# Performance work log

Hardware: AMD Instinct MI355X
Metric: run time of the kernel (lower is better)

Reference implementation:

```python
import jax, jax.numpy as jnp
import numpy as np

N = 4096
IN_F = 512
OUT_F = 256
HEADS = 4
HEAD_DIM = OUT_F // HEADS


def setup_inputs() -> dict:
    key = jax.random.key(0)
    k_feat, k_adj, k_w, k_a = jax.random.split(key, 4)
    features = jax.random.normal(k_feat, (N, IN_F), dtype=jnp.float32)
    adj_matrix = jax.random.uniform(k_adj, (N, N), dtype=jnp.float32)
    # xavier-uniform-ish init scaled small
    W = jax.random.normal(k_w, (OUT_F, IN_F), dtype=jnp.float32) * (1.0 / np.sqrt(IN_F))
    a = jax.random.normal(k_a, (HEADS, 2 * HEAD_DIM), dtype=jnp.float32) * 0.1
    bias = jnp.zeros((OUT_F,), dtype=jnp.float32)
    return {"features": features, "adj_matrix": adj_matrix, "W": W, "a": a, "bias": bias}


def reference(features, adj_matrix, W, a, bias):
    n = features.shape[0]
    h = features @ W.T                      # [N, OUT_F]
    hh = h.reshape(n, HEADS, HEAD_DIM)      # [N, H, D]
    # e[i,j,h] = leaky_relu(<h_i, a[:, :D]> + <h_j, a[:, D:]>) -- additive decomposition
    e_src = jnp.einsum('nhd,hd->nh', hh, a[:, :HEAD_DIM])   # [N, H]
    e_dst = jnp.einsum('nhd,hd->nh', hh, a[:, HEAD_DIM:])   # [N, H]
    e = e_src[:, None, :] + e_dst[None, :, :]               # [N, N, H]
    e = jnp.where(e >= 0, e, 0.2 * e)                       # leaky_relu(0.2)
    mask = adj_matrix[:, :, None] > 0.1                     # [N, N, 1]
    e = jnp.where(mask, e, -jnp.inf)
    attention = jax.nn.softmax(e, axis=1)                   # softmax over j
    attention = jnp.nan_to_num(attention, nan=0.0)          # fully-masked rows -> 0
    attention_mean = attention.mean(axis=2)                 # [N, N]
    h_out = attention_mean @ h + bias                       # [N, OUT_F]
    return h_out
```

## Files before the change

### kernel.cpp

```cpp
#include <hip/hip_runtime.h>
#include <math.h>

#define NN      4096
#define INF_    512
#define OUTF    256
#define NHEAD   4
#define HDIM    64

typedef __attribute__((ext_vector_type(8))) short  short8x;
typedef __attribute__((ext_vector_type(4))) float  float4x;

__device__ __forceinline__ unsigned short f2bf(float x) {
    union { float f; unsigned int u; } c; c.f = x;
    unsigned int r = (c.u + 0x7FFFu + ((c.u >> 16) & 1u)) >> 16;
    return (unsigned short)r;
}
__device__ __forceinline__ float bflo(unsigned int u) {
    union { unsigned int x; float f; } c; c.x = u << 16; return c.f;
}
__device__ __forceinline__ float bfhi(unsigned int u) {
    union { unsigned int x; float f; } c; c.x = u & 0xFFFF0000u; return c.f;
}

__global__ __launch_bounds__(256) void k_cast(const float* __restrict__ feat,
                                              const float* __restrict__ W,
                                              unsigned short* __restrict__ featb,
                                              unsigned short* __restrict__ Wb) {
    const int b = blockIdx.x;
    const float* src;
    unsigned short* dst;
    int idx;
    if (b < 2048) { src = feat; dst = featb; idx = b * 1024 + threadIdx.x * 4; }
    else          { src = W;    dst = Wb;    idx = (b - 2048) * 1024 + threadIdx.x * 4; }
    float4x v = *(const float4x*)(src + idx);
    ushort4 u;
    u.x = f2bf(v[0]); u.y = f2bf(v[1]); u.z = f2bf(v[2]); u.w = f2bf(v[3]);
    *(ushort4*)(dst + idx) = u;
}

__global__ __launch_bounds__(256) void k_h_gemm(const unsigned short* __restrict__ featb,
                                                const unsigned short* __restrict__ Wb,
                                                float* __restrict__ h32,
                                                unsigned short* __restrict__ hT) {
    __shared__ __align__(16) unsigned short lds_f[64 * 40];
    __shared__ __align__(16) unsigned short lds_w[64 * 40];
    const int tid  = threadIdx.x;
    const int w    = tid >> 6;
    const int lane = tid & 63;
    const int lidx = lane & 15;
    const int quad = lane >> 4;
    const int o0 = blockIdx.x * 64;
    const int i0 = blockIdx.y * 64;
    const int sr = tid >> 2;
    const int skq = (tid & 3) * 8;

    float4x acc[4];
    #pragma unroll
    for (int nt = 0; nt < 4; ++nt) acc[nt] = (float4x){0.f, 0.f, 0.f, 0.f};

    ushort4 pf0, pf1, pw0, pw1;
    {
        pf0 = *(const ushort4*)&featb[(size_t)(i0 + sr) * INF_ + skq];
        pf1 = *(const ushort4*)&featb[(size_t)(i0 + sr) * INF_ + skq + 4];
        pw0 = *(const ushort4*)&Wb[(size_t)(o0 + sr) * INF_ + skq];
        pw1 = *(const ushort4*)&Wb[(size_t)(o0 + sr) * INF_ + skq + 4];
    }
    for (int kt = 0; kt < INF_; kt += 32) {
        __syncthreads();
        *(ushort4*)&lds_f[sr * 40 + skq]     = pf0;
        *(ushort4*)&lds_f[sr * 40 + skq + 4] = pf1;
        *(ushort4*)&lds_w[sr * 40 + skq]     = pw0;
        *(ushort4*)&lds_w[sr * 40 + skq + 4] = pw1;
        __syncthreads();
        if (kt + 32 < INF_) {
            int kn = kt + 32;
            pf0 = *(const ushort4*)&featb[(size_t)(i0 + sr) * INF_ + kn + skq];
            pf1 = *(const ushort4*)&featb[(size_t)(i0 + sr) * INF_ + kn + skq + 4];
            pw0 = *(const ushort4*)&Wb[(size_t)(o0 + sr) * INF_ + kn + skq];
            pw1 = *(const ushort4*)&Wb[(size_t)(o0 + sr) * INF_ + kn + skq + 4];
        }
        short8x af = *(const short8x*)&lds_f[(w * 16 + lidx) * 40 + quad * 8];
        short8x bw[4];
        #pragma unroll
        for (int t = 0; t < 4; ++t)
            bw[t] = *(const short8x*)&lds_w[(t * 16 + lidx) * 40 + quad * 8];
        #pragma unroll
        for (int nt = 0; nt < 4; ++nt)
            acc[nt] = __builtin_amdgcn_mfma_f32_16x16x32_bf16(af, bw[nt], acc[nt], 0, 0, 0);
    }
    #pragma unroll
    for (int nt = 0; nt < 4; ++nt) {
        int col = o0 + nt * 16 + lidx;
        int m0r = i0 + w * 16 + quad * 4;
        #pragma unroll
        for (int rr = 0; rr < 4; ++rr)
            h32[(size_t)(m0r + rr) * OUTF + col] = acc[nt][rr];
        ushort4 u;
        u.x = f2bf(acc[nt][0]); u.y = f2bf(acc[nt][1]);
        u.z = f2bf(acc[nt][2]); u.w = f2bf(acc[nt][3]);
        *(ushort4*)&hT[(size_t)col * NN + m0r] = u;
    }
}

__global__ __launch_bounds__(256) void k_edge_proj(const float* __restrict__ h32,
                                                   const float* __restrict__ a,
                                                   float* __restrict__ es,
                                                   unsigned short* __restrict__ Bt,
                                                   unsigned short* __restrict__ Dt) {
    const int n = blockIdx.x;
    const int w = threadIdx.x >> 6;
    const int lane = threadIdx.x & 63;
    float v  = h32[(size_t)n * OUTF + w * HDIM + lane];
    float s1 = v * a[w * 2 * HDIM + lane];
    float s2 = v * a[w * 2 * HDIM + HDIM + lane];
    #pragma unroll
    for (int off = 32; off; off >>= 1) {
        s1 += __shfl_down(s1, off);
        s2 += __shfl_down(s2, off);
    }
    if (lane == 0) {
        es[n * NHEAD + w] = s1;
        Bt[n * NHEAD + w] = f2bf(__expf(s2));
        Dt[n * NHEAD + w] = f2bf(__expf(0.2f * s2));
    }
}

__global__ __launch_bounds__(256) void k_den(const float* __restrict__ adj,
                                             const float* __restrict__ es,
                                             const unsigned short* __restrict__ Bt,
                                             const unsigned short* __restrict__ Dt,
                                             float* __restrict__ coefA,
                                             float* __restrict__ coefC) {
    __shared__ float red[2][2][8];
    const int tid = threadIdx.x;
    const int r  = tid >> 7;
    const int l  = tid & 127;
    const int wv = (tid >> 6) & 1;
    const int i  = blockIdx.x * 2 + r;

    const float4x esv = ((const float4x*)es)[i];
    float TB[4];
    #pragma unroll
    for (int h = 0; h < 4; ++h) TB[h] = __expf(-esv[h]);
    const float4x* arow4 = (const float4x*)(adj + (size_t)i * NN);
    const uint4* B4 = (const uint4*)Bt;
    const uint4* D4 = (const uint4*)Dt;

    float S1[4] = {0.f, 0.f, 0.f, 0.f};
    float S2[4] = {0.f, 0.f, 0.f, 0.f};
    #pragma unroll
    for (int it = 0; it < 8; ++it) {
        int jv = it * 128 + l;
        float4x av = arow4[jv];
        uint4 bu0 = B4[jv * 2], bu1 = B4[jv * 2 + 1];
        uint4 du0 = D4[jv * 2], du1 = D4[jv * 2 + 1];
        const unsigned int* bw = (const unsigned int*)&bu0;
        const unsigned int* dw = (const unsigned int*)&du0;
        (void)bu1; (void)du1;
        unsigned int bwv[8] = {bu0.x, bu0.y, bu0.z, bu0.w, bu1.x, bu1.y, bu1.z, bu1.w};
        unsigned int dwv[8] = {du0.x, du0.y, du0.z, du0.w, du1.x, du1.y, du1.z, du1.w};
        (void)bw; (void)dw;
        #pragma unroll
        for (int u = 0; u < 4; ++u) {
            bool m = av[u] > 0.1f;
            float b0 = bflo(bwv[u * 2]), b1 = bfhi(bwv[u * 2]);
            float b2 = bflo(bwv[u * 2 + 1]), b3 = bfhi(bwv[u * 2 + 1]);
            float d0 = bflo(dwv[u * 2]), d1 = bfhi(dwv[u * 2]);
            float d2 = bflo(dwv[u * 2 + 1]), d3 = bfhi(dwv[u * 2 + 1]);
            bool p0 = b0 >= TB[0], p1 = b1 >= TB[1], p2 = b2 >= TB[2], p3 = b3 >= TB[3];
            S1[0] += (m && p0) ? b0 : 0.f;   S2[0] += (m && !p0) ? d0 : 0.f;
            S1[1] += (m && p1) ? b1 : 0.f;   S2[1] += (m && !p1) ? d1 : 0.f;
            S1[2] += (m && p2) ? b2 : 0.f;   S2[2] += (m && !p2) ? d2 : 0.f;
            S1[3] += (m && p3) ? b3 : 0.f;   S2[3] += (m && !p3) ? d3 : 0.f;
        }
    }
    #pragma unroll
    for (int off = 1; off < 64; off <<= 1) {
        #pragma unroll
        for (int h = 0; h < 4; ++h) {
            S1[h] += __shfl_xor(S1[h], off);
            S2[h] += __shfl_xor(S2[h], off);
        }
    }
    if ((tid & 63) == 0) {
        #pragma unroll
        for (int h = 0; h < 4; ++h) { red[r][wv][h] = S1[h]; red[r][wv][4 + h] = S2[h]; }
    }
    __syncthreads();
    if (tid < 8) {
        int rr = tid >> 2, h = tid & 3;
        int ii = blockIdx.x * 2 + rr;
        float s1 = red[rr][0][h] + red[rr][1][h];
        float s2 = red[rr][0][4 + h] + red[rr][1][4 + h];
        float e = es[ii * NHEAD + h];
        float A = __expf(e), C = __expf(0.2f * e);
        float den = A * s1 + C * s2;
        float sc = den > 0.f ? 0.25f / den : 0.f;
        coefA[ii * NHEAD + h] = A * sc;
        coefC[ii * NHEAD + h] = C * sc;
    }
}

__global__ __launch_bounds__(256) void k_write(const float* __restrict__ adj,
                                               const float* __restrict__ es,
                                               const unsigned short* __restrict__ Bt,
                                               const unsigned short* __restrict__ Dt,
                                               const float* __restrict__ coefA,
                                               const float* __restrict__ coefC,
                                               unsigned short* __restrict__ attn) {
    const int tid = threadIdx.x;
    const int r = tid >> 7;
    const int l = tid & 127;
    const int i = blockIdx.x * 2 + r;

    const float4x esv = ((const float4x*)es)[i];
    const float4x cA = ((const float4x*)coefA)[i];
    const float4x cC = ((const float4x*)coefC)[i];
    float TB[4];
    #pragma unroll
    for (int h = 0; h < 4; ++h) TB[h] = __expf(-esv[h]);
    const float4x* arow4 = (const float4x*)(adj + (size_t)i * NN);
    const uint4* B4 = (const uint4*)Bt;
    const uint4* D4 = (const uint4*)Dt;
    unsigned short* orow = attn + (size_t)i * NN;

    #pragma unroll
    for (int it = 0; it < 8; ++it) {
        int jv = it * 128 + l;
        float4x av = arow4[jv];
        uint4 bu0 = B4[jv * 2], bu1 = B4[jv * 2 + 1];
        uint4 du0 = D4[jv * 2], du1 = D4[jv * 2 + 1];
        unsigned int bwv[8] = {bu0.x, bu0.y, bu0.z, bu0.w, bu1.x, bu1.y, bu1.z, bu1.w};
        unsigned int dwv[8] = {du0.x, du0.y, du0.z, du0.w, du1.x, du1.y, du1.z, du1.w};
        ushort4 o;
        unsigned short* op = (unsigned short*)&o;
        #pragma unroll
        for (int u = 0; u < 4; ++u) {
            float b0 = bflo(bwv[u * 2]), b1 = bfhi(bwv[u * 2]);
            float b2 = bflo(bwv[u * 2 + 1]), b3 = bfhi(bwv[u * 2 + 1]);
            float d0 = bflo(dwv[u * 2]), d1 = bfhi(dwv[u * 2]);
            float d2 = bflo(dwv[u * 2 + 1]), d3 = bfhi(dwv[u * 2 + 1]);
            float p;
            p  = (b0 >= TB[0]) ? cA[0] * b0 : cC[0] * d0;
            p += (b1 >= TB[1]) ? cA[1] * b1 : cC[1] * d1;
            p += (b2 >= TB[2]) ? cA[2] * b2 : cC[2] * d2;
            p += (b3 >= TB[3]) ? cA[3] * b3 : cC[3] * d3;
            op[u] = f2bf((av[u] > 0.1f) ? p : 0.f);
        }
        *(ushort4*)&orow[jv * 4] = o;
    }
}

__global__ __launch_bounds__(256) void k_out_gemm(const unsigned short* __restrict__ attn,
                                                  const unsigned short* __restrict__ hT,
                                                  float* __restrict__ partials) {
    __shared__ __align__(16) unsigned short lds_a[64 * 40];
    __shared__ __align__(16) unsigned short lds_h[256 * 40];
    const int tid  = threadIdx.x;
    const int w    = tid >> 6;
    const int lane = tid & 63;
    const int lidx = lane & 15;
    const int quad = lane >> 4;
    const int i0    = blockIdx.x * 64;
    const int kbase = blockIdx.y * (NN / 4);
    const int srow = tid >> 3;
    const int skq  = tid & 7;

    float4x acc[4][4];
    #pragma unroll
    for (int a = 0; a < 4; ++a)
        #pragma unroll
        for (int b = 0; b < 4; ++b)
            acc[a][b] = (float4x){0.f, 0.f, 0.f, 0.f};

    ushort4 pa[2], ph[8];
    #pragma unroll
    for (int it = 0; it < 2; ++it)
        pa[it] = *(const ushort4*)&attn[(size_t)(i0 + it * 32 + srow) * NN + kbase + skq * 4];
    #pragma unroll
    for (int it = 0; it < 8; ++it)
        ph[it] = *(const ushort4*)&hT[(size_t)(it * 32 + srow) * NN + kbase + skq * 4];

    for (int ks = 0; ks < 32; ++ks) {
        __syncthreads();
        #pragma unroll
        for (int it = 0; it < 2; ++it)
            *(ushort4*)&lds_a[(it * 32 + srow) * 40 + skq * 4] = pa[it];
        #pragma unroll
        for (int it = 0; it < 8; ++it)
            *(ushort4*)&lds_h[(it * 32 + srow) * 40 + skq * 4] = ph[it];
        __syncthreads();
        if (ks < 31) {
            const int ktn = kbase + (ks + 1) * 32;
            #pragma unroll
            for (int it = 0; it < 2; ++it)
                pa[it] = *(const ushort4*)&attn[(size_t)(i0 + it * 32 + srow) * NN + ktn + skq * 4];
            #pragma unroll
            for (int it = 0; it < 8; ++it)
                ph[it] = *(const ushort4*)&hT[(size_t)(it * 32 + srow) * NN + ktn + skq * 4];
        }
        short8x af[4], bfr[4];
        #pragma unroll
        for (int t = 0; t < 4; ++t) {
            af[t]  = *(const short8x*)&lds_a[(t * 16 + lidx) * 40 + quad * 8];
            bfr[t] = *(const short8x*)&lds_h[(w * 64 + t * 16 + lidx) * 40 + quad * 8];
        }
        #pragma unroll
        for (int it = 0; it < 4; ++it)
            #pragma unroll
            for (int nt = 0; nt < 4; ++nt)
                acc[it][nt] = __builtin_amdgcn_mfma_f32_16x16x32_bf16(
                    af[it], bfr[nt], acc[it][nt], 0, 0, 0);
    }
    float* pbase = partials + (size_t)blockIdx.y * NN * OUTF;
    #pragma unroll
    for (int it = 0; it < 4; ++it)
        #pragma unroll
        for (int nt = 0; nt < 4; ++nt)
            #pragma unroll
            for (int rr = 0; rr < 4; ++rr) {
                int row = i0 + it * 16 + quad * 4 + rr;
                int col = w * 64 + nt * 16 + lidx;
                pbase[(size_t)row * OUTF + col] = acc[it][nt][rr];
            }
}

__global__ __launch_bounds__(256) void k_reduce_out(const float* __restrict__ partials,
                                                    const float* __restrict__ bias,
                                                    float* __restrict__ out) {
    const int i = blockIdx.x;
    const int n = threadIdx.x;
    float acc = bias[n];
    #pragma unroll
    for (int s = 0; s < 4; ++s)
        acc += partials[((size_t)s * NN + i) * OUTF + n];
    out[(size_t)i * OUTF + n] = acc;
}

extern "C" void kernel_launch(void* const* d_in, const int* in_sizes, int n_in,
                              void* d_out, int out_size, void* d_ws, size_t ws_size,
                              hipStream_t stream) {
    const float* feat = (const float*)d_in[0];
    const float* adj  = (const float*)d_in[1];
    const float* W    = (const float*)d_in[2];
    const float* a    = (const float*)d_in[3];
    const float* bias = (const float*)d_in[4];
    float* out = (float*)d_out;

    char* ws = (char*)d_ws;
    float*          es    = (float*)(ws + 0);
    unsigned short* Btb   = (unsigned short*)(ws + (64u << 10));
    unsigned short* Dtb   = (unsigned short*)(ws + (96u << 10));
    float*          coefA = (float*)(ws + (128u << 10));
    float*          coefC = (float*)(ws + (192u << 10));
    unsigned short* hT    = (unsigned short*)(ws + (256u << 10));
    unsigned short* attn  = (unsigned short*)(ws + (2560u << 10));
    unsigned short* featb = (unsigned short*)(ws + (2560u << 10));
    unsigned short* Wb    = (unsigned short*)(ws + (6656u << 10));
    float*          h32   = (float*)(ws + (7168u << 10));
    float*          partials = (float*)(ws + (35328u << 10));

    k_cast      <<<2176,        256, 0, stream>>>(feat, W, featb, Wb);
    k_h_gemm    <<<dim3(4, 64), 256, 0, stream>>>(featb, Wb, h32, hT);
    k_edge_proj <<<NN,          256, 0, stream>>>(h32, a, es, Btb, Dtb);
    k_den       <<<2048,        256, 0, stream>>>(adj, es, Btb, Dtb, coefA, coefC);
    k_write     <<<2048,        256, 0, stream>>>(adj, es, Btb, Dtb, coefA, coefC, attn);
    k_out_gemm  <<<dim3(64, 4), 256, 0, stream>>>(attn, hT, partials);
    k_reduce_out<<<NN,          256, 0, stream>>>(partials, bias, out);
}
```

Measured before the change: 190.0 us.

## Fold attention vector into W, fuse denominator and write passes, deepen split-K

Precomputes W^T·a per head so the edge scores come straight from the features, dropping the fp32 h buffer and the separate edge-projection kernel. Merges the softmax-denominator and attention-write kernels into one, keeping the coefficients in shared memory, so the coefA/coefC global round trip and one launch go away. Doubles the split-K factor of the output GEMM to 8 for more parallelism, at the cost of a larger partials reduction. The edge scores now use fp32 features rather than h, which slightly changes the rounding of the scores.

Measured after the change: 184.0 us. 3.2% less time.

```diff
diff --git a/kernel.cpp b/kernel.cpp
--- a/kernel.cpp
+++ b/kernel.cpp
@@ -6,6 +6,7 @@
 #define OUTF    256
 #define NHEAD   4
 #define HDIM    64
+#define KSPLIT  8
 
 typedef __attribute__((ext_vector_type(8))) short  short8x;
 typedef __attribute__((ext_vector_type(4))) float  float4x;
@@ -22,25 +23,78 @@
     union { unsigned int x; float f; } c; c.x = u & 0xFFFF0000u; return c.f;
 }
 
-__global__ __launch_bounds__(256) void k_cast(const float* __restrict__ feat,
+__global__ __launch_bounds__(256) void k_prep(const float* __restrict__ feat,
                                               const float* __restrict__ W,
+                                              const float* __restrict__ a,
                                               unsigned short* __restrict__ featb,
-                                              unsigned short* __restrict__ Wb) {
+                                              unsigned short* __restrict__ Wb,
+                                              float* __restrict__ wsrc,
+                                              float* __restrict__ wdst) {
     const int b = blockIdx.x;
+    if (b < 8) {
+        const int kk = threadIdx.x & 63, h = threadIdx.x >> 6;
+        const int k = b * 64 + kk;
+        float s = 0.f, d2 = 0.f;
+        #pragma unroll 8
+        for (int d = 0; d < 64; ++d) {
+            float wv = W[(size_t)(h * HDIM + d) * INF_ + k];
+            s  += wv * a[h * 2 * HDIM + d];
+            d2 += wv * a[h * 2 * HDIM + HDIM + d];
+        }
+        wsrc[k * NHEAD + h] = s;
+        wdst[k * NHEAD + h] = d2;
+        return;
+    }
+    const int bb = b - 8;
     const float* src;
     unsigned short* dst;
     int idx;
-    if (b < 2048) { src = feat; dst = featb; idx = b * 1024 + threadIdx.x * 4; }
-    else          { src = W;    dst = Wb;    idx = (b - 2048) * 1024 + threadIdx.x * 4; }
+    if (bb < 2048) { src = feat; dst = featb; idx = bb * 1024 + threadIdx.x * 4; }
+    else           { src = W;    dst = Wb;    idx = (bb - 2048) * 1024 + threadIdx.x * 4; }
     float4x v = *(const float4x*)(src + idx);
     ushort4 u;
     u.x = f2bf(v[0]); u.y = f2bf(v[1]); u.z = f2bf(v[2]); u.w = f2bf(v[3]);
     *(ushort4*)(dst + idx) = u;
 }
 
+__global__ __launch_bounds__(256) void k_edge(const float* __restrict__ feat,
+                                              const float* __restrict__ wsrc,
+                                              const float* __restrict__ wdst,
+                                              float* __restrict__ es,
+                                              unsigned short* __restrict__ Bt,
+                                              unsigned short* __restrict__ Dt) {
+    const int r = blockIdx.x * 16 + (threadIdx.x >> 4);
+    const int lane = threadIdx.x & 15;
+    float s[4] = {0.f, 0.f, 0.f, 0.f};
+    float d[4] = {0.f, 0.f, 0.f, 0.f};
+    for (int kk = 0; kk < 32; ++kk) {
+        int k = kk * 16 + lane;
+        float f = feat[(size_t)r * INF_ + k];
+        float4x ws = ((const float4x*)wsrc)[k];
+        float4x wd = ((const float4x*)wdst)[k];
+        #pragma unroll
+        for (int h = 0; h < 4; ++h) { s[h] += f * ws[h]; d[h] += f * wd[h]; }
+    }
+    #pragma unroll
+    for (int off = 1; off < 16; off <<= 1) {
+        #pragma unroll
+        for (int h = 0; h < 4; ++h) {
+            s[h] += __shfl_xor(s[h], off);
+            d[h] += __shfl_xor(d[h], off);
+        }
+    }
+    if (lane == 0) {
+        #pragma unroll
+        for (int h = 0; h < 4; ++h) {
+            es[r * NHEAD + h] = s[h];
+            Bt[r * NHEAD + h] = f2bf(__expf(d[h]));
+            Dt[r * NHEAD + h] = f2bf(__expf(0.2f * d[h]));
+        }
+    }
+}
+
 __global__ __launch_bounds__(256) void k_h_gemm(const unsigned short* __restrict__ featb,
                                                 const unsigned short* __restrict__ Wb,
-                                                float* __restrict__ h32,
                                                 unsigned short* __restrict__ hT) {
     __shared__ __align__(16) unsigned short lds_f[64 * 40];
     __shared__ __align__(16) unsigned short lds_w[64 * 40];
@@ -58,13 +112,11 @@
     #pragma unroll
     for (int nt = 0; nt < 4; ++nt) acc[nt] = (float4x){0.f, 0.f, 0.f, 0.f};
 
-    ushort4 pf0, pf1, pw0, pw1;
-    {
-        pf0 = *(const ushort4*)&featb[(size_t)(i0 + sr) * INF_ + skq];
-        pf1 = *(const ushort4*)&featb[(size_t)(i0 + sr) * INF_ + skq + 4];
-        pw0 = *(const ushort4*)&Wb[(size_t)(o0 + sr) * INF_ + skq];
-        pw1 = *(const ushort4*)&Wb[(size_t)(o0 + sr) * INF_ + skq + 4];
-    }
+    ushort4 pf0 = *(const ushort4*)&featb[(size_t)(i0 + sr) * INF_ + skq];
+    ushort4 pf1 = *(const ushort4*)&featb[(size_t)(i0 + sr) * INF_ + skq + 4];
+    ushort4 pw0 = *(const ushort4*)&Wb[(size_t)(o0 + sr) * INF_ + skq];
+    ushort4 pw1 = *(const ushort4*)&Wb[(size_t)(o0 + sr) * INF_ + skq + 4];
+
     for (int kt = 0; kt < INF_; kt += 32) {
         __syncthreads();
         *(ushort4*)&lds_f[sr * 40 + skq]     = pf0;
@@ -92,9 +144,6 @@
     for (int nt = 0; nt < 4; ++nt) {
         int col = o0 + nt * 16 + lidx;
         int m0r = i0 + w * 16 + quad * 4;
-        #pragma unroll
-        for (int rr = 0; rr < 4; ++rr)
-            h32[(size_t)(m0r + rr) * OUTF + col] = acc[nt][rr];
         ushort4 u;
         u.x = f2bf(acc[nt][0]); u.y = f2bf(acc[nt][1]);
         u.z = f2bf(acc[nt][2]); u.w = f2bf(acc[nt][3]);
@@ -102,36 +151,13 @@
     }
 }
 
-__global__ __launch_bounds__(256) void k_edge_proj(const float* __restrict__ h32,
-                                                   const float* __restrict__ a,
-                                                   float* __restrict__ es,
-                                                   unsigned short* __restrict__ Bt,
-                                                   unsigned short* __restrict__ Dt) {
-    const int n = blockIdx.x;
-    const int w = threadIdx.x >> 6;
-    const int lane = threadIdx.x & 63;
-    float v  = h32[(size_t)n * OUTF + w * HDIM + lane];
-    float s1 = v * a[w * 2 * HDIM + lane];
-    float s2 = v * a[w * 2 * HDIM + HDIM + lane];
-    #pragma unroll
-    for (int off = 32; off; off >>= 1) {
-        s1 += __shfl_down(s1, off);
-        s2 += __shfl_down(s2, off);
-    }
-    if (lane == 0) {
-        es[n * NHEAD + w] = s1;
-        Bt[n * NHEAD + w] = f2bf(__expf(s2));
-        Dt[n * NHEAD + w] = f2bf(__expf(0.2f * s2));
-    }
-}
-
-__global__ __launch_bounds__(256) void k_den(const float* __restrict__ adj,
-                                             const float* __restrict__ es,
-                                             const unsigned short* __restrict__ Bt,
-                                             const unsigned short* __restrict__ Dt,
-                                             float* __restrict__ coefA,
-                                             float* __restrict__ coefC) {
+__global__ __launch_bounds__(256) void k_attn(const float* __restrict__ adj,
+                                              const float* __restrict__ es,
+                                              const unsigned short* __restrict__ Bt,
+                                              const unsigned short* __restrict__ Dt,
+                                              unsigned short* __restrict__ attn) {
     __shared__ float red[2][2][8];
+    __shared__ float cfs[2][8];
     const int tid = threadIdx.x;
     const int r  = tid >> 7;
     const int l  = tid & 127;
@@ -154,12 +180,8 @@
         float4x av = arow4[jv];
         uint4 bu0 = B4[jv * 2], bu1 = B4[jv * 2 + 1];
         uint4 du0 = D4[jv * 2], du1 = D4[jv * 2 + 1];
-        const unsigned int* bw = (const unsigned int*)&bu0;
-        const unsigned int* dw = (const unsigned int*)&du0;
-        (void)bu1; (void)du1;
         unsigned int bwv[8] = {bu0.x, bu0.y, bu0.z, bu0.w, bu1.x, bu1.y, bu1.z, bu1.w};
         unsigned int dwv[8] = {du0.x, du0.y, du0.z, du0.w, du1.x, du1.y, du1.z, du1.w};
-        (void)bw; (void)dw;
         #pragma unroll
         for (int u = 0; u < 4; ++u) {
             bool m = av[u] > 0.1f;
@@ -196,34 +218,15 @@
         float A = __expf(e), C = __expf(0.2f * e);
         float den = A * s1 + C * s2;
         float sc = den > 0.f ? 0.25f / den : 0.f;
-        coefA[ii * NHEAD + h] = A * sc;
-        coefC[ii * NHEAD + h] = C * sc;
-    }
-}
-
-__global__ __launch_bounds__(256) void k_write(const float* __restrict__ adj,
-                                               const float* __restrict__ es,
-                                               const unsigned short* __restrict__ Bt,
-                                               const unsigned short* __restrict__ Dt,
-                                               const float* __restrict__ coefA,
-                                               const float* __restrict__ coefC,
-                                               unsigned short* __restrict__ attn) {
-    const int tid = threadIdx.x;
-    const int r = tid >> 7;
-    const int l = tid & 127;
-    const int i = blockIdx.x * 2 + r;
-
-    const float4x esv = ((const float4x*)es)[i];
-    const float4x cA = ((const float4x*)coefA)[i];
-    const float4x cC = ((const float4x*)coefC)[i];
-    float TB[4];
-    #pragma unroll
-    for (int h = 0; h < 4; ++h) TB[h] = __expf(-esv[h]);
-    const float4x* arow4 = (const float4x*)(adj + (size_t)i * NN);
-    const uint4* B4 = (const uint4*)Bt;
-    const uint4* D4 = (const uint4*)Dt;
+        cfs[rr][h]     = A * sc;
+        cfs[rr][4 + h] = C * sc;
+    }
+    __syncthreads();
+    float cA[4], cC[4];
+    #pragma unroll
+    for (int h = 0; h < 4; ++h) { cA[h] = cfs[r][h]; cC[h] = cfs[r][4 + h]; }
+
     unsigned short* orow = attn + (size_t)i * NN;
-
     #pragma unroll
     for (int it = 0; it < 8; ++it) {
         int jv = it * 128 + l;
@@ -262,7 +265,7 @@
     const int lidx = lane & 15;
     const int quad = lane >> 4;
     const int i0    = blockIdx.x * 64;
-    const int kbase = blockIdx.y * (NN / 4);
+    const int kbase = blockIdx.y * (NN / KSPLIT);
     const int srow = tid >> 3;
     const int skq  = tid & 7;
 
@@ -281,7 +284,8 @@
     for (int it = 0; it < 8; ++it)
         ph[it] = *(const ushort4*)&hT[(size_t)(it * 32 + srow) * NN + kbase + skq * 4];
 
-    for (int ks = 0; ks < 32; ++ks) {
+    const int KSTEPS = (NN / KSPLIT) / 32;
+    for (int ks = 0; ks < KSTEPS; ++ks) {
         __syncthreads();
         #pragma unroll
         for (int it = 0; it < 2; ++it)
@@ -290,7 +294,7 @@
         for (int it = 0; it < 8; ++it)
             *(ushort4*)&lds_h[(it * 32 + srow) * 40 + skq * 4] = ph[it];
         __syncthreads();
-        if (ks < 31) {
+        if (ks < KSTEPS - 1) {
             const int ktn = kbase + (ks + 1) * 32;
             #pragma unroll
             for (int it = 0; it < 2; ++it)
@@ -332,7 +336,7 @@
     const int n = threadIdx.x;
     float acc = bias[n];
     #pragma unroll
-    for (int s = 0; s < 4; ++s)
+    for (int s = 0; s < KSPLIT; ++s)
         acc += partials[((size_t)s * NN + i) * OUTF + n];
     out[(size_t)i * OUTF + n] = acc;
 }
@@ -351,20 +355,18 @@
     float*          es    = (float*)(ws + 0);
     unsigned short* Btb   = (unsigned short*)(ws + (64u << 10));
     unsigned short* Dtb   = (unsigned short*)(ws + (96u << 10));
-    float*          coefA = (float*)(ws + (128u << 10));
-    float*          coefC = (float*)(ws + (192u << 10));
+    float*          wsrc  = (float*)(ws + (128u << 10));
+    float*          wdst  = (float*)(ws + (160u << 10));
     unsigned short* hT    = (unsigned short*)(ws + (256u << 10));
     unsigned short* attn  = (unsigned short*)(ws + (2560u << 10));
     unsigned short* featb = (unsigned short*)(ws + (2560u << 10));
     unsigned short* Wb    = (unsigned short*)(ws + (6656u << 10));
-    float*          h32   = (float*)(ws + (7168u << 10));
     float*          partials = (float*)(ws + (35328u << 10));
 
-    k_cast      <<<2176,        256, 0, stream>>>(feat, W, featb, Wb);
-    k_h_gemm    <<<dim3(4, 64), 256, 0, stream>>>(featb, Wb, h32, hT);
-    k_edge_proj <<<NN,          256, 0, stream>>>(h32, a, es, Btb, Dtb);
-    k_den       <<<2048,        256, 0, stream>>>(adj, es, Btb, Dtb, coefA, coefC);
-    k_write     <<<2048,        256, 0, stream>>>(adj, es, Btb, Dtb, coefA, coefC, attn);
-    k_out_gemm  <<<dim3(64, 4), 256, 0, stream>>>(attn, hT, partials);
-    k_reduce_out<<<NN,          256, 0, stream>>>(partials, bias, out);
-}
+    k_prep      <<<2184,             256, 0, stream>>>(feat, W, a, featb, Wb, wsrc, wdst);
+    k_edge      <<<256,              256, 0, stream>>>(feat, wsrc, wdst, es, Btb, Dtb);
+    k_h_gemm    <<<dim3(4, 64),      256, 0, stream>>>(featb, Wb, hT);
+    k_attn      <<<2048,             256, 0, stream>>>(adj, es, Btb, Dtb, attn);
+    k_out_gemm  <<<dim3(64, KSPLIT), 256, 0, stream>>>(attn, hT, partials);
+    k_reduce_out<<<NN,               256, 0, stream>>>(partials, bias, out);
+}
```
